# Optimization experiments

Measured on AMD Instinct MI355X. Metric: run time of the kernel, lower is better.

## Reference

```python
import jax, jax.numpy as jnp
import numpy as np

B, PRE, POST = 32, 2048, 2048
TAU_PRE = 2.0
TAU_POST = 2.0
V_TH = 1.0  # IF-neuron firing threshold


def setup_inputs() -> dict:
    key = jax.random.key(0)
    k1, k2, k3, k4 = jax.random.split(key, 4)
    # input spikes are binary (Bernoulli p=0.2)
    x = (jax.random.uniform(k1, (B, PRE)) < 0.2).astype(jnp.float32)
    # Linear weight [post, pre], Kaiming-ish scale
    W = jax.random.normal(k2, (POST, PRE), dtype=jnp.float32) / np.sqrt(PRE)
    # pre/post traces carried over from previous timesteps
    trace_pre = jax.random.uniform(k3, (B, PRE), dtype=jnp.float32)
    trace_post = jax.random.uniform(k4, (B, POST), dtype=jnp.float32)
    return {"x": x, "W": W, "trace_pre": trace_pre, "trace_post": trace_post}


def reference(x, W, trace_pre, trace_post):
    # connection: i = x @ W^T  -> [B, POST]
    i = x @ W.T
    # node: IF neuron, Heaviside spike
    spike = (i >= V_TH).astype(x.dtype)
    # trace decay (EMA) + spike accumulation
    tp = trace_pre - trace_pre / TAU_PRE + x        # [B, PRE]
    tq = trace_post - trace_post / TAU_POST + spike  # [B, POST]
    # clamp weight once; batch outer-product sums expressed as GEMMs
    Wc = jnp.clip(W, -1.0, 1.0)
    dw = (-Wc * jnp.einsum('bp,bq->pq', tq, x)
          + Wc * jnp.einsum('bp,bq->pq', spike, tp))  # [POST, PRE]
    return (spike, dw)
```

## Files before the change

### kernel.cpp

```cpp
#include <hip/hip_runtime.h>

#define B_ 32
#define PRE_ 2048
#define POST_ 2048
#define QT 8
#define WPAD 2056

typedef __attribute__((ext_vector_type(8))) short short8;
typedef __attribute__((ext_vector_type(4))) short short4v;
typedef __attribute__((ext_vector_type(4))) float floatx4;

__device__ __forceinline__ unsigned short f2bf(float f) {
    unsigned u = __float_as_uint(f);
    u += 0x7FFF + ((u >> 16) & 1);
    return (unsigned short)(u >> 16);
}
__device__ __forceinline__ float bf2f(unsigned short h) {
    return __uint_as_float(((unsigned)h) << 16);
}


__global__ __launch_bounds__(256) void stdp_prep(
    const float* __restrict__ x, const float* __restrict__ tpre,
    unsigned short* __restrict__ ws)
{
    int lin = blockIdx.x * 256 + threadIdx.x;
    int base = lin * 4;
    floatx4 xv = *(const floatx4*)(x + base);
    short4v xr;
#pragma unroll
    for (int j = 0; j < 4; ++j)
        xr[j] = (short)(__float_as_uint(xv[j]) >> 16);
    *(short4v*)(ws + base) = xr;

    int p  = lin >> 3;
    int b0 = (lin & 7) * 4;
    short4v tpv, xcv;
#pragma unroll
    for (int j = 0; j < 4; ++j) {
        float xx = x[(b0 + j) * PRE_ + p];
        float tt = tpre[(b0 + j) * PRE_ + p];
        tpv[j] = (short)f2bf(0.5f * tt + xx);
        xcv[j] = (short)(__float_as_uint(xx) >> 16);
    }
    *(short4v*)(ws + 65536 + p * 64 + b0) = tpv;
    *(short4v*)(ws + 65536 + p * 64 + 32 + b0) = xcv;
}

__global__ __launch_bounds__(512) void stdp_fused(
    const float* __restrict__ W, const float* __restrict__ trace_post,
    const unsigned short* __restrict__ ws, float* __restrict__ out)
{
    __shared__ __align__(16) unsigned short Wh[QT * WPAD];
    __shared__ __align__(16) unsigned short Wl[QT * WPAD];
    __shared__ __align__(16) float red[8 * 2 * 4 * 64];
    __shared__ __align__(16) unsigned short spnq[QT * 64];

    const int tid  = threadIdx.x;
    const int wave = tid >> 6, lane = tid & 63;
    const int quad = lane >> 4, l16 = lane & 15;
    const int q0   = blockIdx.x * QT;
    const int qb   = l16 & 7;
    const int kbase = wave * 256;

    float tpr[4];
    if (wave < 2 && l16 < QT) {
#pragma unroll
        for (int r = 0; r < 4; ++r)
            tpr[r] = trace_post[(wave * 16 + quad * 4 + r) * POST_ + q0 + l16];
    }

    floatx4 wv[8];
#pragma unroll
    for (int r = 0; r < 8; ++r)
        wv[r] = *(const floatx4*)(W + (q0 + r) * PRE_ + kbase + lane * 4);
#pragma unroll
    for (int r = 0; r < 8; ++r) {
        short4v hv, lv;
#pragma unroll
        for (int j = 0; j < 4; ++j) {
            unsigned short h = f2bf(wv[r][j]);
            hv[j] = (short)h;
            lv[j] = (short)f2bf(wv[r][j] - bf2f(h));
        }
        *(short4v*)&Wh[r * WPAD + kbase + lane * 4] = hv;
        *(short4v*)&Wl[r * WPAD + kbase + lane * 4] = lv;
    }

    const unsigned short* xrow = ws;
    floatx4 acc0 = {0.f, 0.f, 0.f, 0.f};
    floatx4 acc1 = {0.f, 0.f, 0.f, 0.f};
#pragma unroll
    for (int s = 0; s < 8; ++s) {
        int ko = kbase + s * 32 + quad * 8;
        short8 a0 = *(const short8*)(xrow + l16 * PRE_ + ko);
        short8 a1 = *(const short8*)(xrow + (16 + l16) * PRE_ + ko);
        short8 bh = *(const short8*)(Wh + qb * WPAD + ko);
        short8 bl = *(const short8*)(Wl + qb * WPAD + ko);
        acc0 = __builtin_amdgcn_mfma_f32_16x16x32_bf16(a0, bh, acc0, 0, 0, 0);
        acc0 = __builtin_amdgcn_mfma_f32_16x16x32_bf16(a0, bl, acc0, 0, 0, 0);
        acc1 = __builtin_amdgcn_mfma_f32_16x16x32_bf16(a1, bh, acc1, 0, 0, 0);
        acc1 = __builtin_amdgcn_mfma_f32_16x16x32_bf16(a1, bl, acc1, 0, 0, 0);
    }

    const unsigned short* frag = ws + 65536;
    const int pbase = wave * 256;
    short8 ftp = *(const short8*)(frag + (pbase + l16) * 64 + quad * 8);
    short8 fx  = *(const short8*)(frag + (pbase + l16) * 64 + 32 + quad * 8);

#pragma unroll
    for (int r = 0; r < 4; ++r) {
        red[((wave * 2 + 0) * 4 + r) * 64 + lane] = acc0[r];
        red[((wave * 2 + 1) * 4 + r) * 64 + lane] = acc1[r];
    }
    __syncthreads();

    if (wave < 2 && l16 < QT) {
        int q = q0 + l16;
#pragma unroll
        for (int r = 0; r < 4; ++r) {
            float s = 0.f;
#pragma unroll
            for (int w = 0; w < 8; ++w) s += red[((w * 2 + wave) * 4 + r) * 64 + lane];
            int b = wave * 16 + quad * 4 + r;
            float spike = (s >= 1.0f) ? 1.0f : 0.0f;
            out[b * POST_ + q] = spike;
            float ntq = -(0.5f * tpr[r] + spike);
            spnq[l16 * 64 + b]      = f2bf(spike);
            spnq[l16 * 64 + 32 + b] = f2bf(ntq);
        }
    }
    __syncthreads();

    short8 fs  = *(const short8*)(spnq + qb * 64 + quad * 8);
    short8 fnq = *(const short8*)(spnq + qb * 64 + 32 + quad * 8);
    float* dw = out + B_ * POST_;

#pragma unroll 4
    for (int it = 0; it < 16; ++it) {
        int pn = (pbase + (((it + 1) & 15) * 16) + l16) * 64;
        short8 ntp = *(const short8*)(frag + pn + quad * 8);
        short8 nx  = *(const short8*)(frag + pn + 32 + quad * 8);

        floatx4 acc = {0.f, 0.f, 0.f, 0.f};
        acc = __builtin_amdgcn_mfma_f32_16x16x32_bf16(fs,  ftp, acc, 0, 0, 0);
        acc = __builtin_amdgcn_mfma_f32_16x16x32_bf16(fnq, fx,  acc, 0, 0, 0);

        int p = pbase + it * 16 + l16;
        if (quad < 2) {
#pragma unroll
            for (int r = 0; r < 4; ++r) {
                int qd = quad * 4 + r;
                float wvv = bf2f(Wh[qd * WPAD + p]) + bf2f(Wl[qd * WPAD + p]);
                wvv = fminf(fmaxf(wvv, -1.0f), 1.0f);
                dw[(q0 + qd) * PRE_ + p] = wvv * acc[r];
            }
        }
        ftp = ntp; fx = nx;
    }
}

extern "C" void kernel_launch(void* const* d_in, const int* in_sizes, int n_in,
                              void* d_out, int out_size, void* d_ws, size_t ws_size,
                              hipStream_t stream) {
    const float* x     = (const float*)d_in[0];
    const float* W     = (const float*)d_in[1];
    const float* tpre  = (const float*)d_in[2];
    const float* tpost = (const float*)d_in[3];
    float* out = (float*)d_out;
    unsigned short* ws = (unsigned short*)d_ws;

    hipLaunchKernelGGL(stdp_prep, dim3(64), dim3(256), 0, stream, x, tpre, ws);
    hipLaunchKernelGGL(stdp_fused, dim3(POST_ / QT), dim3(512), 0, stream,
                       W, tpost, ws, out);
}
```

Measured before the change: 92.82 us.

## Split fused kernel into forward and dw kernels with coalesced dw stores

Splits the fused kernel into a forward kernel (spike GEMM, QT halved to 4 for more blocks) and a separate dw kernel that writes its spike and neg-trace fragments to workspace. The dw kernel swaps the MFMA operand order so each lane stores float4 rows contiguously, and it re-reads W from global memory instead of using the LDS hi/lo split. The prep kernel now transposes through LDS so its reads are coalesced. The cost is an extra launch and a second pass over W, in exchange for more parallelism and wider dw writes.

```diff
diff --git a/kernel.cpp b/kernel.cpp
--- a/kernel.cpp
+++ b/kernel.cpp
@@ -3,8 +3,12 @@
 #define B_ 32
 #define PRE_ 2048
 #define POST_ 2048
-#define QT 8
+#define QT 4
 #define WPAD 2056
+
+#define XROW_OFF 0
+#define FRAG_OFF 65536
+#define SPQ_OFF  196608
 
 typedef __attribute__((ext_vector_type(8))) short short8;
 typedef __attribute__((ext_vector_type(4))) short short4v;
@@ -19,63 +23,60 @@
     return __uint_as_float(((unsigned)h) << 16);
 }
 
-
-__global__ __launch_bounds__(256) void stdp_prep(
+__global__ __launch_bounds__(64) void stdp_prep(
     const float* __restrict__ x, const float* __restrict__ tpre,
     unsigned short* __restrict__ ws)
 {
-    int lin = blockIdx.x * 256 + threadIdx.x;
-    int base = lin * 4;
-    floatx4 xv = *(const floatx4*)(x + base);
+    __shared__ __align__(16) unsigned short tt[8 * 80];
+    const int lane = threadIdx.x;
+    const int p0 = blockIdx.x * 8;
+    const int b = lane >> 1, c4 = (lane & 1) * 4;
+
+    floatx4 xv = *(const floatx4*)(x    + b * PRE_ + p0 + c4);
+    floatx4 tv = *(const floatx4*)(tpre + b * PRE_ + p0 + c4);
     short4v xr;
 #pragma unroll
-    for (int j = 0; j < 4; ++j)
+    for (int j = 0; j < 4; ++j) {
         xr[j] = (short)(__float_as_uint(xv[j]) >> 16);
-    *(short4v*)(ws + base) = xr;
-
-    int p  = lin >> 3;
-    int b0 = (lin & 7) * 4;
-    short4v tpv, xcv;
-#pragma unroll
-    for (int j = 0; j < 4; ++j) {
-        float xx = x[(b0 + j) * PRE_ + p];
-        float tt = tpre[(b0 + j) * PRE_ + p];
-        tpv[j] = (short)f2bf(0.5f * tt + xx);
-        xcv[j] = (short)(__float_as_uint(xx) >> 16);
+        tt[(c4 + j) * 80 + b]      = f2bf(0.5f * tv[j] + xv[j]);
+        tt[(c4 + j) * 80 + 32 + b] = (unsigned short)xr[j];
     }
-    *(short4v*)(ws + 65536 + p * 64 + b0) = tpv;
-    *(short4v*)(ws + 65536 + p * 64 + 32 + b0) = xcv;
+    *(short4v*)(ws + XROW_OFF + b * PRE_ + p0 + c4) = xr;
+    __syncthreads();
+    const int pp = lane >> 3, seg = lane & 7;
+    short8 v = *(const short8*)(tt + pp * 80 + seg * 8);
+    *(short8*)(ws + FRAG_OFF + (p0 + pp) * 64 + seg * 8) = v;
 }
 
-__global__ __launch_bounds__(512) void stdp_fused(
-    const float* __restrict__ W, const float* __restrict__ trace_post,
-    const unsigned short* __restrict__ ws, float* __restrict__ out)
+__global__ __launch_bounds__(512) void stdp_fwd(
+    const float* __restrict__ W, const float* __restrict__ tpost,
+    unsigned short* __restrict__ ws, float* __restrict__ out)
 {
-    __shared__ __align__(16) unsigned short Wh[QT * WPAD];
-    __shared__ __align__(16) unsigned short Wl[QT * WPAD];
-    __shared__ __align__(16) float red[8 * 2 * 4 * 64];
-    __shared__ __align__(16) unsigned short spnq[QT * 64];
+    __shared__ __align__(16) unsigned short sh[2 * QT * WPAD];
+    unsigned short* Wh = sh;
+    unsigned short* Wl = sh + QT * WPAD;
+    float* red = (float*)sh;
 
     const int tid  = threadIdx.x;
     const int wave = tid >> 6, lane = tid & 63;
     const int quad = lane >> 4, l16 = lane & 15;
     const int q0   = blockIdx.x * QT;
-    const int qb   = l16 & 7;
+    const int qb   = l16 & (QT - 1);
     const int kbase = wave * 256;
 
     float tpr[4];
     if (wave < 2 && l16 < QT) {
 #pragma unroll
         for (int r = 0; r < 4; ++r)
-            tpr[r] = trace_post[(wave * 16 + quad * 4 + r) * POST_ + q0 + l16];
+            tpr[r] = tpost[(wave * 16 + quad * 4 + r) * POST_ + q0 + l16];
     }
 
-    floatx4 wv[8];
+    floatx4 wv[QT];
 #pragma unroll
-    for (int r = 0; r < 8; ++r)
+    for (int r = 0; r < QT; ++r)
         wv[r] = *(const floatx4*)(W + (q0 + r) * PRE_ + kbase + lane * 4);
 #pragma unroll
-    for (int r = 0; r < 8; ++r) {
+    for (int r = 0; r < QT; ++r) {
         short4v hv, lv;
 #pragma unroll
         for (int j = 0; j < 4; ++j) {
@@ -87,7 +88,7 @@
         *(short4v*)&Wl[r * WPAD + kbase + lane * 4] = lv;
     }
 
-    const unsigned short* xrow = ws;
+    const unsigned short* xrow = ws + XROW_OFF;
     floatx4 acc0 = {0.f, 0.f, 0.f, 0.f};
     floatx4 acc1 = {0.f, 0.f, 0.f, 0.f};
 #pragma unroll
@@ -103,11 +104,7 @@
         acc1 = __builtin_amdgcn_mfma_f32_16x16x32_bf16(a1, bl, acc1, 0, 0, 0);
     }
 
-    const unsigned short* frag = ws + 65536;
-    const int pbase = wave * 256;
-    short8 ftp = *(const short8*)(frag + (pbase + l16) * 64 + quad * 8);
-    short8 fx  = *(const short8*)(frag + (pbase + l16) * 64 + 32 + quad * 8);
-
+    __syncthreads();
 #pragma unroll
     for (int r = 0; r < 4; ++r) {
         red[((wave * 2 + 0) * 4 + r) * 64 + lane] = acc0[r];
@@ -116,6 +113,7 @@
     __syncthreads();
 
     if (wave < 2 && l16 < QT) {
+        unsigned short* spq = ws + SPQ_OFF;
         int q = q0 + l16;
 #pragma unroll
         for (int r = 0; r < 4; ++r) {
@@ -126,37 +124,49 @@
             float spike = (s >= 1.0f) ? 1.0f : 0.0f;
             out[b * POST_ + q] = spike;
             float ntq = -(0.5f * tpr[r] + spike);
-            spnq[l16 * 64 + b]      = f2bf(spike);
-            spnq[l16 * 64 + 32 + b] = f2bf(ntq);
+            spq[q * 64 + b]      = f2bf(spike);
+            spq[q * 64 + 32 + b] = f2bf(ntq);
         }
     }
-    __syncthreads();
+}
 
-    short8 fs  = *(const short8*)(spnq + qb * 64 + quad * 8);
-    short8 fnq = *(const short8*)(spnq + qb * 64 + 32 + quad * 8);
+__global__ __launch_bounds__(256) void stdp_dw(
+    const float* __restrict__ W, const unsigned short* __restrict__ ws,
+    float* __restrict__ out)
+{
+    const unsigned short* frag = ws + FRAG_OFF;
+    const unsigned short* spq  = ws + SPQ_OFF;
     float* dw = out + B_ * POST_;
 
-#pragma unroll 4
-    for (int it = 0; it < 16; ++it) {
-        int pn = (pbase + (((it + 1) & 15) * 16) + l16) * 64;
-        short8 ntp = *(const short8*)(frag + pn + quad * 8);
-        short8 nx  = *(const short8*)(frag + pn + 32 + quad * 8);
+    const int tid  = threadIdx.x;
+    const int wave = tid >> 6, lane = tid & 63;
+    const int quad = lane >> 4, l16 = lane & 15;
+    const int wid = (blockIdx.x & 7) * 128 + (blockIdx.x >> 3);
+    const int gw  = wid * 4 + wave;
+    const int qt  = gw >> 5;
+    const int ps  = gw & 31;
+    const int q   = qt * 16 + l16;
+    const int p0  = ps * 64;
 
+    short8 fsp = *(const short8*)(spq + q * 64 + quad * 8);
+    short8 fnq = *(const short8*)(spq + q * 64 + 32 + quad * 8);
+
+#pragma unroll
+    for (int it = 0; it < 4; ++it) {
+        int p = p0 + it * 16;
+        short8 ftp = *(const short8*)(frag + (p + l16) * 64 + quad * 8);
+        short8 fx  = *(const short8*)(frag + (p + l16) * 64 + 32 + quad * 8);
         floatx4 acc = {0.f, 0.f, 0.f, 0.f};
-        acc = __builtin_amdgcn_mfma_f32_16x16x32_bf16(fs,  ftp, acc, 0, 0, 0);
-        acc = __builtin_amdgcn_mfma_f32_16x16x32_bf16(fnq, fx,  acc, 0, 0, 0);
-
-        int p = pbase + it * 16 + l16;
-        if (quad < 2) {
+        acc = __builtin_amdgcn_mfma_f32_16x16x32_bf16(ftp, fsp, acc, 0, 0, 0);
+        acc = __builtin_amdgcn_mfma_f32_16x16x32_bf16(fx,  fnq, acc, 0, 0, 0);
+        floatx4 wq = *(const floatx4*)(W + q * PRE_ + p + quad * 4);
+        floatx4 o;
 #pragma unroll
-            for (int r = 0; r < 4; ++r) {
-                int qd = quad * 4 + r;
-                float wvv = bf2f(Wh[qd * WPAD + p]) + bf2f(Wl[qd * WPAD + p]);
-                wvv = fminf(fmaxf(wvv, -1.0f), 1.0f);
-                dw[(q0 + qd) * PRE_ + p] = wvv * acc[r];
-            }
+        for (int r = 0; r < 4; ++r) {
+            float wc = fminf(fmaxf(wq[r], -1.0f), 1.0f);
+            o[r] = wc * acc[r];
         }
-        ftp = ntp; fx = nx;
+        *(floatx4*)(dw + q * PRE_ + p + quad * 4) = o;
     }
 }
 
@@ -170,7 +180,8 @@
     float* out = (float*)d_out;
     unsigned short* ws = (unsigned short*)d_ws;
 
-    hipLaunchKernelGGL(stdp_prep, dim3(64), dim3(256), 0, stream, x, tpre, ws);
-    hipLaunchKernelGGL(stdp_fused, dim3(POST_ / QT), dim3(512), 0, stream,
+    hipLaunchKernelGGL(stdp_prep, dim3(256), dim3(64), 0, stream, x, tpre, ws);
+    hipLaunchKernelGGL(stdp_fwd,  dim3(POST_ / QT), dim3(512), 0, stream,
                        W, tpost, ws, out);
+    hipLaunchKernelGGL(stdp_dw,   dim3(1024), dim3(256), 0, stream, W, ws, out);
 }
```

Result: slower. 96.88 us (+4.4%).
